# Performance work log

Hardware: AMD Instinct MI355X
Metric: run time of the kernel (lower is better)

Reference implementation:

```python
import jax, jax.numpy as jnp
import numpy as np

ND, NA, E, EL, H, F = 100000, 50000, 500000, 200000, 128, 128


def setup_inputs() -> dict:
    key = jax.random.key(0)
    ks = jax.random.split(key, 20)
    def W(k, shape):
        return jax.random.normal(k, shape, dtype=jnp.float32) * 0.05
    inp = {
        'doc_x': jax.random.normal(ks[0], (ND, F), dtype=jnp.float32),
        'author_node_id': jnp.arange(NA, dtype=jnp.int64 if jax.config.jax_enable_x64 else jnp.int32),
        'edge_index': jnp.stack([
            jax.random.randint(ks[1], (E,), 0, ND),   # doc src
            jax.random.randint(ks[2], (E,), 0, NA),   # author dst
        ]),
        'edge_label_index': jnp.stack([
            jax.random.randint(ks[3], (EL,), 0, ND),
            jax.random.randint(ks[4], (EL,), 0, NA),
        ]),
        'doc_lin_W': W(ks[5], (F, H)), 'doc_lin_b': W(ks[6], (H,)),
        'author_emb': W(ks[7], (NA, H)),
        'c1_da_Wl': W(ks[8], (H, H)), 'c1_da_bl': W(ks[9], (H,)), 'c1_da_Wr': W(ks[10], (H, H)),
        'c1_ad_Wl': W(ks[11], (H, H)), 'c1_ad_bl': W(ks[12], (H,)), 'c1_ad_Wr': W(ks[13], (H, H)),
        'c2_da_Wl': W(ks[14], (H, H)), 'c2_da_bl': W(ks[15], (H,)), 'c2_da_Wr': W(ks[16], (H, H)),
        'c2_ad_Wl': W(ks[17], (H, H)), 'c2_ad_bl': W(ks[18], (H,)), 'c2_ad_Wr': W(ks[19], (H, H)),
    }
    return inp


def sage(x_src, x_dst, src, dst, num_dst, Wl, bl, Wr):
    # PyG SAGEConv (aggr='mean'): lin_l(mean_j x_src[j]) + lin_r(x_dst)
    msg = x_src[src]                                            # [E, H]
    agg = jax.ops.segment_sum(msg, dst, num_segments=num_dst)   # [num_dst, H]
    deg = jax.ops.segment_sum(jnp.ones_like(dst, dtype=x_src.dtype), dst, num_segments=num_dst)
    agg = agg / jnp.maximum(deg, 1.0)[:, None]
    return agg @ Wl + bl + x_dst @ Wr


def reference(doc_x, author_node_id, edge_index, edge_label_index,
              doc_lin_W, doc_lin_b, author_emb,
              c1_da_Wl, c1_da_bl, c1_da_Wr, c1_ad_Wl, c1_ad_bl, c1_ad_Wr,
              c2_da_Wl, c2_da_bl, c2_da_Wr, c2_ad_Wl, c2_ad_bl, c2_ad_Wr):
    x_doc = doc_x @ doc_lin_W + doc_lin_b          # [ND, H]
    x_author = author_emb[author_node_id]          # [NA, H]
    src_d, dst_a = edge_index[0], edge_index[1]
    # layer 1 (per-edge-type convs, to_hetero semantics) + ReLU
    h_a = sage(x_doc, x_author, src_d, dst_a, NA, c1_da_Wl, c1_da_bl, c1_da_Wr)
    h_d = sage(x_author, x_doc, dst_a, src_d, ND, c1_ad_Wl, c1_ad_bl, c1_ad_Wr)
    h_a, h_d = jax.nn.relu(h_a), jax.nn.relu(h_d)
    # layer 2
    o_a = sage(h_d, h_a, src_d, dst_a, NA, c2_da_Wl, c2_da_bl, c2_da_Wr)
    o_d = sage(h_a, h_d, dst_a, src_d, ND, c2_ad_Wl, c2_ad_bl, c2_ad_Wr)
    # edge scorer: dot product of gathered endpoint embeddings
    pred = (o_d[edge_label_index[0]] * o_a[edge_label_index[1]]).sum(-1)  # [EL]
    return pred
```

## Files before the change

kernel.cpp:

```cpp
#include <hip/hip_runtime.h>

typedef unsigned short u16;
typedef __attribute__((ext_vector_type(8))) short vbf16x8;
typedef __attribute__((ext_vector_type(4))) float vf32x4;

__device__ __forceinline__ float bf2f(u16 u) {
    union { unsigned int i; float f; } v; v.i = ((unsigned int)u) << 16; return v.f;
}
__device__ __forceinline__ u16 f2bf(float f) {
    union { float f; unsigned int i; } v; v.f = f;
    return (u16)((v.i + 0x7fffu + ((v.i >> 16) & 1u)) >> 16);
}

struct TPack { const float* src[9]; u16* dst[9]; };

#define NBUK 256
#define NBLK_BIN 256
#define SCAP 24
#define OVFCAP 32768
#define PACK_SH 17

__global__ __launch_bounds__(256) void wtp(TPack p, int* __restrict__ ovfn) {
    int b = blockIdx.x;
    if (b == 0 && threadIdx.x < 2) ovfn[threadIdx.x] = 0;
    int mat = b >> 6;
    const float* s = p.src[mat];
    u16* d = p.dst[mat];
    int i = (b & 63) * 256 + threadIdx.x;
    int k = i >> 7, n = i & 127;
    d[(size_t)n * 128 + k] = f2bf(s[(size_t)k * 128 + n]);
}

__global__ __launch_bounds__(256) void mega2(
    const float* __restrict__ A1f, const u16* __restrict__ W1T,
    const float* __restrict__ biasd, u16* __restrict__ xdoc, int M, int BD,
    const float* __restrict__ emb, const int* __restrict__ ids,
    u16* __restrict__ xauth, int NA, int gatherB,
    const int* __restrict__ src, const int* __restrict__ dst,
    unsigned* __restrict__ stageD, unsigned* __restrict__ stageA,
    int* __restrict__ cntD, int* __restrict__ cntA,
    uint2* __restrict__ ovfD, uint2* __restrict__ ovfA, int* __restrict__ ovfn,
    int E, int shD, int shA) {
    __shared__ u16 WS[128 * 128];
    const int tid = threadIdx.x;

    const long b = blockIdx.x;
    const long nB = 2 * NBLK_BIN;
    const long T = (long)BD + nB + gatherB;
    const long gq0 = (b * BD) / T, gq1 = ((b + 1) * BD) / T;

    if (gq1 > gq0) {
        const int tile = (int)gq0;
        const int lane = tid & 63, wave = tid >> 6;
        const int r15 = lane & 15, kq = lane >> 4;
        const int rowbase = tile * 128 + wave * 32;
        const int m0 = rowbase + r15, m1 = rowbase + 16 + r15;
        const bool v0 = rowbase < M, v1 = rowbase + 16 < M;

        vf32x4 acc0[8], acc1[8];
#pragma unroll
        for (int i = 0; i < 8; ++i) { acc0[i] = (vf32x4)(0.0f); acc1[i] = (vf32x4)(0.0f); }

#pragma unroll
        for (int i = 0; i < 8; ++i) {
            int L = i * 256 + tid;
            int n = L >> 4, bk = L & 15;
            *(uint4*)(WS + ((size_t)n * 16 + (bk ^ (n & 15))) * 8) =
                *(const uint4*)(W1T + (size_t)L * 8);
        }
        __syncthreads();

#pragma unroll
        for (int ks = 0; ks < 4; ++ks) {
            vbf16x8 a0 = (vbf16x8)(short)0, a1 = (vbf16x8)(short)0;
            if (v0) {
                const float* p = A1f + (size_t)m0 * 128 + ks * 32 + kq * 8;
                float4 lo = *(const float4*)p, hi = *(const float4*)(p + 4);
                a0[0] = (short)f2bf(lo.x); a0[1] = (short)f2bf(lo.y);
                a0[2] = (short)f2bf(lo.z); a0[3] = (short)f2bf(lo.w);
                a0[4] = (short)f2bf(hi.x); a0[5] = (short)f2bf(hi.y);
                a0[6] = (short)f2bf(hi.z); a0[7] = (short)f2bf(hi.w);
            }
            if (v1) {
                const float* p = A1f + (size_t)m1 * 128 + ks * 32 + kq * 8;
                float4 lo = *(const float4*)p, hi = *(const float4*)(p + 4);
                a1[0] = (short)f2bf(lo.x); a1[1] = (short)f2bf(lo.y);
                a1[2] = (short)f2bf(lo.z); a1[3] = (short)f2bf(lo.w);
                a1[4] = (short)f2bf(hi.x); a1[5] = (short)f2bf(hi.y);
                a1[6] = (short)f2bf(hi.z); a1[7] = (short)f2bf(hi.w);
            }
#pragma unroll
            for (int nt = 0; nt < 8; ++nt) {
                vbf16x8 bb = *(const vbf16x8*)(
                    WS + ((size_t)(nt * 16 + r15) * 16 + ((ks * 4 + kq) ^ r15)) * 8);
                acc0[nt] = __builtin_amdgcn_mfma_f32_16x16x32_bf16(a0, bb, acc0[nt], 0, 0, 0);
                acc1[nt] = __builtin_amdgcn_mfma_f32_16x16x32_bf16(a1, bb, acc1[nt], 0, 0, 0);
            }
        }

#pragma unroll
        for (int nt = 0; nt < 8; ++nt) {
            const float bv = biasd[nt * 16 + r15];
#pragma unroll
            for (int r = 0; r < 4; ++r) {
                if (v0) xdoc[(size_t)(rowbase + kq * 4 + r) * 128 + nt * 16 + r15] =
                    f2bf(acc0[nt][r] + bv);
                if (v1) xdoc[(size_t)(rowbase + 16 + kq * 4 + r) * 128 + nt * 16 + r15] =
                    f2bf(acc1[nt][r] + bv);
            }
        }
        return;
    }

    const long b2 = b - gq0;
    const long T2 = T - BD;
    const long bq0 = (b2 * nB) / T2, bq1 = ((b2 + 1) * nB) / T2;

    if (bq1 > bq0) {
        int* lcnt = (int*)WS;
        int bb = (int)bq0;
        const bool isD = bb < NBLK_BIN;
        const int blk = isD ? bb : bb - NBLK_BIN;
        const int* key = isD ? src : dst;
        const int* val = isD ? dst : src;
        const int shift = isD ? shD : shA;
        unsigned* stage = isD ? stageD : stageA;
        int* cnt = isD ? cntD : cntA;
        uint2* ovf = isD ? ovfD : ovfA;
        int* on = ovfn + (isD ? 0 : 1);
        const int per = (E + NBLK_BIN - 1) / NBLK_BIN;
        const int beg = blk * per;
        const int end = min(beg + per, E);
        for (int i = tid; i < NBUK; i += 256) lcnt[i] = 0;
        __syncthreads();
        for (int e = beg + tid; e < end; e += 256) {
            int k = key[e], v = val[e];
            int bkt = k >> shift;
            int slot = atomicAdd(&lcnt[bkt], 1);
            if (slot < SCAP) {
                unsigned local = (unsigned)(k - (bkt << shift));
                stage[((size_t)bkt * NBLK_BIN + blk) * SCAP + slot] =
                    (local << PACK_SH) | (unsigned)v;
            } else {
                int oi = atomicAdd(on, 1);
                if (oi < OVFCAP) ovf[oi] = make_uint2((unsigned)k, (unsigned)v);
            }
        }
        __syncthreads();
        for (int i = tid; i < NBUK; i += 256)
            cnt[(size_t)i * NBLK_BIN + blk] = min(lcnt[i], SCAP);
        return;
    }

    int gid = (int)(b2 - bq0) * 256 + tid;
    if (gid >= NA * 16) return;
    int n = gid >> 4, f = gid & 15;
    int id = ids[n];
    const float* s = emb + (size_t)id * 128 + f * 8;
    float4 lo = *(const float4*)(s);
    float4 hi = *(const float4*)(s + 4);
    u16 o[8] = {f2bf(lo.x), f2bf(lo.y), f2bf(lo.z), f2bf(lo.w),
                f2bf(hi.x), f2bf(hi.y), f2bf(hi.z), f2bf(hi.w)};
    *(uint4*)(xauth + (size_t)n * 128 + f * 8) = *(const uint4*)o;
}

__global__ __launch_bounds__(256) void bucket_count2(
    const unsigned* __restrict__ stageD, const unsigned* __restrict__ stageA,
    const int* __restrict__ cntD, const int* __restrict__ cntA,
    const uint2* __restrict__ ovfD, const uint2* __restrict__ ovfA,
    const int* __restrict__ ovfn,
    int* __restrict__ cnt_d, int* __restrict__ cnt_a, int* __restrict__ btot,
    int ND, int NA, int shD, int shA) {
    __shared__ int hist[1024];
    __shared__ int segc[NBLK_BIN];
    __shared__ int red[256];
    const bool isD = (int)blockIdx.x < NBUK;
    const int b = isD ? (int)blockIdx.x : (int)blockIdx.x - NBUK;
    const int sh = isD ? shD : shA;
    const int N = isD ? ND : NA;
    const int base = b << sh;
    const int range = min(1 << sh, N - base);
    const int tid = threadIdx.x;
    if (range <= 0) { if (tid == 0) btot[blockIdx.x] = 0; return; }
    const unsigned* stage = (isD ? stageD : stageA) + (size_t)b * NBLK_BIN * SCAP;
    const int* scnt = (isD ? cntD : cntA) + (size_t)b * NBLK_BIN;
    const uint2* ovf = isD ? ovfD : ovfA;
    const int nov = min(ovfn[isD ? 0 : 1], OVFCAP);
    int* out = isD ? cnt_d : cnt_a;
    for (int i = tid; i < (1 << sh); i += 256) hist[i] = 0;
    segc[tid] = scnt[tid];
    __syncthreads();
    int my = 0;
    for (int j = tid; j < NBLK_BIN * SCAP; j += 256) {
        int seg = j / SCAP, slot = j - seg * SCAP;
        if (slot < segc[seg]) { atomicAdd(&hist[stage[j] >> PACK_SH], 1); ++my; }
    }
    for (int i = tid; i < nov; i += 256) {
        int k = (int)ovf[i].x;
        if ((k >> sh) == b) { atomicAdd(&hist[k - base], 1); ++my; }
    }
    red[tid] = my;
    __syncthreads();
    for (int s = 128; s > 0; s >>= 1) {
        if (tid < s) red[tid] += red[tid + s];
        __syncthreads();
    }
    if (tid == 0) btot[blockIdx.x] = red[0];
    for (int i = tid; i < range; i += 256) out[base + i] = hist[i];
}

__global__ __launch_bounds__(256) void bucket_fill3(
    const unsigned* __restrict__ stageD, const unsigned* __restrict__ stageA,
    const int* __restrict__ cntD, const int* __restrict__ cntA,
    const uint2* __restrict__ ovfD, const uint2* __restrict__ ovfA,
    const int* __restrict__ ovfn,
    const int* __restrict__ cnt_d, const int* __restrict__ cnt_a,
    const int* __restrict__ btot,
    int* __restrict__ offs_d, int* __restrict__ offs_a,
    int* __restrict__ nbr_d, int* __restrict__ nbr_a,
    int ND, int NA, int shD, int shA) {
    __shared__ int lcur[1024];
    __shared__ int segc[NBLK_BIN];
    __shared__ int sh[256];
    __shared__ int carry;
    const bool isD = (int)blockIdx.x < NBUK;
    const int b = isD ? (int)blockIdx.x : (int)blockIdx.x - NBUK;
    const int shft = isD ? shD : shA;
    const int N = isD ? ND : NA;
    const int base = b << shft;
    const int range = min(1 << shft, N - base);
    if (range <= 0) return;
    const unsigned* stage = (isD ? stageD : stageA) + (size_t)b * NBLK_BIN * SCAP;
    const int* scnt = (isD ? cntD : cntA) + (size_t)b * NBLK_BIN;
    const uint2* ovf = isD ? ovfD : ovfA;
    const int nov = min(ovfn[isD ? 0 : 1], OVFCAP);
    const int* cnodes = isD ? cnt_d : cnt_a;
    int* offs = isD ? offs_d : offs_a;
    int* nbr = isD ? nbr_d : nbr_a;
    const int tid = threadIdx.x;
    segc[tid] = scnt[tid];
    {
        const int lo = isD ? 0 : NBUK;
        int acc = 0;
        for (int j = lo + tid; j < (int)blockIdx.x; j += 256) acc += btot[j];
        sh[tid] = acc;
        __syncthreads();
        for (int s = 128; s > 0; s >>= 1) {
            if (tid < s) sh[tid] += sh[tid + s];
            __syncthreads();
        }
        if (tid == 0) carry = sh[0];
        __syncthreads();
    }
    for (int c0 = 0; c0 < range; c0 += 256) {
        int i = c0 + tid;
        int v = (i < range) ? cnodes[base + i] : 0;
        sh[tid] = v;
        __syncthreads();
        for (int off = 1; off < 256; off <<= 1) {
            int t = tid >= off ? sh[tid - off] : 0;
            __syncthreads();
            sh[tid] += t;
            __syncthreads();
        }
        if (i < range) {
            int ex = carry + sh[tid] - v;
            lcur[i] = ex;
            offs[base + i] = ex;
        }
        __syncthreads();
        if (tid == 255) carry += sh[255];
        __syncthreads();
    }
    if (tid == 0) offs[base + range] = carry;
    __syncthreads();
    for (int j = tid; j < NBLK_BIN * SCAP; j += 256) {
        int seg = j / SCAP, slot = j - seg * SCAP;
        if (slot < segc[seg]) {
            unsigned pk = stage[j];
            int local = pk >> PACK_SH;
            int v = (int)(pk & ((1u << PACK_SH) - 1u));
            nbr[atomicAdd(&lcur[local], 1)] = v;
        }
    }
    for (int i = tid; i < nov; i += 256) {
        int k = (int)ovf[i].x;
        if ((k >> shft) == b)
            nbr[atomicAdd(&lcur[k - base], 1)] = (int)ovf[i].y;
    }
}

__global__ __launch_bounds__(256) void agg_mean2(
    const u16* __restrict__ xa, const int* __restrict__ offs_a,
    const int* __restrict__ nbr_a, u16* __restrict__ outa, int NA,
    const u16* __restrict__ xd, const int* __restrict__ offs_d,
    const int* __restrict__ nbr_d, u16* __restrict__ outd, int ND) {
    int gid = blockIdx.x * 256 + threadIdx.x;
    int node = gid >> 4, f = gid & 15;
    int lane = threadIdx.x & 63;
    int gbase = lane & 48;
    const u16* x; const int* offs; const int* nbr; u16* out;
    if (node < NA) { x = xa; offs = offs_a; nbr = nbr_a; out = outa; }
    else {
        node -= NA;
        if (node >= ND) return;
        x = xd; offs = offs_d; nbr = nbr_d; out = outd;
    }
    int beg = offs[node], end = offs[node + 1];
    float acc[8] = {0, 0, 0, 0, 0, 0, 0, 0};

    for (int i = beg; i < end; i += 16) {
        int cnt = end - i; if (cnt > 16) cnt = 16;
        int myn = (i + f < end) ? nbr[i + f] : 0;
        int t = 0;
        for (; t + 3 < cnt; t += 4) {
            int i0 = __shfl(myn, gbase + t);
            int i1 = __shfl(myn, gbase + t + 1);
            int i2 = __shfl(myn, gbase + t + 2);
            int i3 = __shfl(myn, gbase + t + 3);
            uint4 q0 = *(const uint4*)(x + (size_t)i0 * 128 + f * 8);
            uint4 q1 = *(const uint4*)(x + (size_t)i1 * 128 + f * 8);
            uint4 q2 = *(const uint4*)(x + (size_t)i2 * 128 + f * 8);
            uint4 q3 = *(const uint4*)(x + (size_t)i3 * 128 + f * 8);
            acc[0] += bf2f((u16)(q0.x & 0xffff)) + bf2f((u16)(q1.x & 0xffff))
                    + bf2f((u16)(q2.x & 0xffff)) + bf2f((u16)(q3.x & 0xffff));
            acc[1] += bf2f((u16)(q0.x >> 16))    + bf2f((u16)(q1.x >> 16))
                    + bf2f((u16)(q2.x >> 16))    + bf2f((u16)(q3.x >> 16));
            acc[2] += bf2f((u16)(q0.y & 0xffff)) + bf2f((u16)(q1.y & 0xffff))
                    + bf2f((u16)(q2.y & 0xffff)) + bf2f((u16)(q3.y & 0xffff));
            acc[3] += bf2f((u16)(q0.y >> 16))    + bf2f((u16)(q1.y >> 16))
                    + bf2f((u16)(q2.y >> 16))    + bf2f((u16)(q3.y >> 16));
            acc[4] += bf2f((u16)(q0.z & 0xffff)) + bf2f((u16)(q1.z & 0xffff))
                    + bf2f((u16)(q2.z & 0xffff)) + bf2f((u16)(q3.z & 0xffff));
            acc[5] += bf2f((u16)(q0.z >> 16))    + bf2f((u16)(q1.z >> 16))
                    + bf2f((u16)(q2.z >> 16))    + bf2f((u16)(q3.z >> 16));
            acc[6] += bf2f((u16)(q0.w & 0xffff)) + bf2f((u16)(q1.w & 0xffff))
                    + bf2f((u16)(q2.w & 0xffff)) + bf2f((u16)(q3.w & 0xffff));
            acc[7] += bf2f((u16)(q0.w >> 16))    + bf2f((u16)(q1.w >> 16))
                    + bf2f((u16)(q2.w >> 16))    + bf2f((u16)(q3.w >> 16));
        }
        for (; t < cnt; ++t) {
            int i0 = __shfl(myn, gbase + t);
            uint4 q0 = *(const uint4*)(x + (size_t)i0 * 128 + f * 8);
            acc[0] += bf2f((u16)(q0.x & 0xffff));
            acc[1] += bf2f((u16)(q0.x >> 16));
            acc[2] += bf2f((u16)(q0.y & 0xffff));
            acc[3] += bf2f((u16)(q0.y >> 16));
            acc[4] += bf2f((u16)(q0.z & 0xffff));
            acc[5] += bf2f((u16)(q0.z >> 16));
            acc[6] += bf2f((u16)(q0.w & 0xffff));
            acc[7] += bf2f((u16)(q0.w >> 16));
        }
    }
    float inv = 1.0f / fmaxf((float)(end - beg), 1.0f);
    u16 o[8];
#pragma unroll
    for (int j = 0; j < 8; ++j) o[j] = f2bf(acc[j] * inv);
    *(uint4*)(out + (size_t)node * 128 + f * 8) = *(const uint4*)o;
}

struct SideParams3 {
    const u16* A1b; const u16* W1T;
    const u16* A2b; const u16* W2T;
    const float* bias; u16* out;
    int M; int do_relu; int ntiles; int gblocks;
};
__global__ __launch_bounds__(256) void conv_gemm3(SideParams3 sa, SideParams3 sd) {
    __shared__ u16 WS[2 * 128 * 128];
    const bool isA = (int)blockIdx.x < sa.gblocks;
    SideParams3 P = isA ? sa : sd;
    const int gb = isA ? (int)blockIdx.x : (int)blockIdx.x - sa.gblocks;
    const int tid = threadIdx.x;
    const int lane = tid & 63, wave = tid >> 6;
    const int r15 = lane & 15, kq = lane >> 4;

#pragma unroll
    for (int i = 0; i < 8; ++i) {
        int L = i * 256 + tid;
        int n = L >> 4, bk = L & 15;
        *(uint4*)(WS + ((size_t)n * 16 + (bk ^ (n & 15))) * 8) =
            *(const uint4*)(P.W1T + (size_t)L * 8);
        *(uint4*)(WS + 16384 + ((size_t)n * 16 + (bk ^ (n & 15))) * 8) =
            *(const uint4*)(P.W2T + (size_t)L * 8);
    }
    __syncthreads();
    float bv[8];
#pragma unroll
    for (int nt = 0; nt < 8; ++nt) bv[nt] = P.bias[nt * 16 + r15];

    auto loadA = [&](const u16* Ab, int tile, vbf16x8* fa, vbf16x8* fb) {
        const int rowbase = tile * 128 + wave * 32;
        const int m0 = rowbase + r15, m1 = rowbase + 16 + r15;
        const bool v0 = rowbase < P.M, v1 = rowbase + 16 < P.M;
#pragma unroll
        for (int ks = 0; ks < 4; ++ks) {
            fa[ks] = v0 ? *(const vbf16x8*)(Ab + (size_t)m0 * 128 + ks * 32 + kq * 8)
                        : (vbf16x8)(short)0;
            fb[ks] = v1 ? *(const vbf16x8*)(Ab + (size_t)m1 * 128 + ks * 32 + kq * 8)
                        : (vbf16x8)(short)0;
        }
    };

    vbf16x8 c1a[4], c1b[4], c2a[4], c2b[4], n1a[4], n1b[4];
    if (gb < P.ntiles) loadA(P.A1b, gb, c1a, c1b);
    for (int t = gb; t < P.ntiles; t += P.gblocks) {
        loadA(P.A2b, t, c2a, c2b);
        const int tn = t + P.gblocks;
        if (tn < P.ntiles) loadA(P.A1b, tn, n1a, n1b);

        vf32x4 acc0[8], acc1[8];
#pragma unroll
        for (int i = 0; i < 8; ++i) { acc0[i] = (vf32x4)(0.0f); acc1[i] = (vf32x4)(0.0f); }
#pragma unroll
        for (int ks = 0; ks < 4; ++ks) {
#pragma unroll
            for (int nt = 0; nt < 8; ++nt) {
                vbf16x8 b = *(const vbf16x8*)(
                    WS + ((size_t)(nt * 16 + r15) * 16 + ((ks * 4 + kq) ^ r15)) * 8);
                acc0[nt] = __builtin_amdgcn_mfma_f32_16x16x32_bf16(c1a[ks], b, acc0[nt], 0, 0, 0);
                acc1[nt] = __builtin_amdgcn_mfma_f32_16x16x32_bf16(c1b[ks], b, acc1[nt], 0, 0, 0);
            }
        }
#pragma unroll
        for (int ks = 0; ks < 4; ++ks) {
#pragma unroll
            for (int nt = 0; nt < 8; ++nt) {
                vbf16x8 b = *(const vbf16x8*)(
                    WS + 16384 + ((size_t)(nt * 16 + r15) * 16 + ((ks * 4 + kq) ^ r15)) * 8);
                acc0[nt] = __builtin_amdgcn_mfma_f32_16x16x32_bf16(c2a[ks], b, acc0[nt], 0, 0, 0);
                acc1[nt] = __builtin_amdgcn_mfma_f32_16x16x32_bf16(c2b[ks], b, acc1[nt], 0, 0, 0);
            }
        }

        const int rowbase = t * 128 + wave * 32;
        const bool v0 = rowbase < P.M, v1 = rowbase + 16 < P.M;
#pragma unroll
        for (int nt = 0; nt < 8; ++nt) {
#pragma unroll
            for (int r = 0; r < 4; ++r) {
                if (v0) {
                    float v = acc0[nt][r] + bv[nt];
                    if (P.do_relu) v = fmaxf(v, 0.0f);
                    P.out[(size_t)(rowbase + kq * 4 + r) * 128 + nt * 16 + r15] = f2bf(v);
                }
                if (v1) {
                    float v = acc1[nt][r] + bv[nt];
                    if (P.do_relu) v = fmaxf(v, 0.0f);
                    P.out[(size_t)(rowbase + 16 + kq * 4 + r) * 128 + nt * 16 + r15] = f2bf(v);
                }
            }
        }
#pragma unroll
        for (int ks = 0; ks < 4; ++ks) { c1a[ks] = n1a[ks]; c1b[ks] = n1b[ks]; }
    }
}

__global__ __launch_bounds__(256) void edge_dot(
    const u16* __restrict__ od, const u16* __restrict__ oa,
    const int* __restrict__ i0, const int* __restrict__ i1,
    float* __restrict__ pred, int EL) {
    int gid = blockIdx.x * 256 + threadIdx.x;
    if (gid >= EL * 16) return;
    int e = gid >> 4, f = gid & 15;
    uint4 x = *(const uint4*)(od + (size_t)i0[e] * 128 + f * 8);
    uint4 y = *(const uint4*)(oa + (size_t)i1[e] * 128 + f * 8);
    float s = 0.0f;
    s += bf2f((u16)(x.x & 0xffff)) * bf2f((u16)(y.x & 0xffff));
    s += bf2f((u16)(x.x >> 16))    * bf2f((u16)(y.x >> 16));
    s += bf2f((u16)(x.y & 0xffff)) * bf2f((u16)(y.y & 0xffff));
    s += bf2f((u16)(x.y >> 16))    * bf2f((u16)(y.y >> 16));
    s += bf2f((u16)(x.z & 0xffff)) * bf2f((u16)(y.z & 0xffff));
    s += bf2f((u16)(x.z >> 16))    * bf2f((u16)(y.z >> 16));
    s += bf2f((u16)(x.w & 0xffff)) * bf2f((u16)(y.w & 0xffff));
    s += bf2f((u16)(x.w >> 16))    * bf2f((u16)(y.w >> 16));
    s += __shfl_xor(s, 1);
    s += __shfl_xor(s, 2);
    s += __shfl_xor(s, 4);
    s += __shfl_xor(s, 8);
    if (f == 0) pred[e] = s;
}

extern "C" void kernel_launch(void* const* d_in, const int* in_sizes, int n_in,
                              void* d_out, int out_size, void* d_ws, size_t ws_size,
                              hipStream_t stream) {
    const float* doc_x    = (const float*)d_in[0];
    const int*   auth_id  = (const int*)d_in[1];
    const int*   eidx     = (const int*)d_in[2];
    const int*   elidx    = (const int*)d_in[3];
    const float* W_doc    = (const float*)d_in[4];
    const float* b_doc    = (const float*)d_in[5];
    const float* emb      = (const float*)d_in[6];
    const float* c1_da_Wl = (const float*)d_in[7];
    const float* c1_da_bl = (const float*)d_in[8];
    const float* c1_da_Wr = (const float*)d_in[9];
    const float* c1_ad_Wl = (const float*)d_in[10];
    const float* c1_ad_bl = (const float*)d_in[11];
    const float* c1_ad_Wr = (const float*)d_in[12];
    const float* c2_da_Wl = (const float*)d_in[13];
    const float* c2_da_bl = (const float*)d_in[14];
    const float* c2_da_Wr = (const float*)d_in[15];
    const float* c2_ad_Wl = (const float*)d_in[16];
    const float* c2_ad_bl = (const float*)d_in[17];
    const float* c2_ad_Wr = (const float*)d_in[18];

    const int ND = in_sizes[0] / 128;
    const int NA = in_sizes[1];
    const int E  = in_sizes[2] / 2;
    const int EL = in_sizes[3] / 2;
    const int* e_src = eidx;
    const int* e_dst = eidx + E;
    const int BA = (NA + 127) / 128, BD = (ND + 127) / 128;
    const int gatherB = (NA * 16 + 255) / 256;

    char* base = (char*)d_ws;
    size_t off = 0;
    auto alloc = [&](size_t bytes) {
        void* p = base + off;
        off = (off + bytes + 255) & ~(size_t)255;
        return p;
    };
    u16*  xdoc  = (u16*)alloc((size_t)ND * 128 * 2);
    u16*  xauth = (u16*)alloc((size_t)NA * 128 * 2);
    u16*  hd    = (u16*)alloc((size_t)ND * 128 * 2);
    u16*  ha    = (u16*)alloc((size_t)NA * 128 * 2);
    u16*  aggA  = (u16*)alloc((size_t)NA * 128 * 2);
    u16*  aggD  = (u16*)alloc((size_t)ND * 128 * 2);
    u16*  wt    = (u16*)alloc((size_t)9 * 128 * 128 * 2);
    int*  cnt   = (int*)alloc((size_t)(ND + NA) * 4);
    int*  offs_d = (int*)alloc((size_t)(ND + 1) * 4);
    int*  offs_a = (int*)alloc((size_t)(NA + 1) * 4);
    int*  nbr_d = (int*)alloc((size_t)E * 4);
    int*  nbr_a = (int*)alloc((size_t)E * 4);
    int*  cntD  = (int*)alloc((size_t)NBUK * NBLK_BIN * 4);
    int*  cntA  = (int*)alloc((size_t)NBUK * NBLK_BIN * 4);
    int*  btot  = (int*)alloc((size_t)2 * NBUK * 4);
    uint2* ovfD = (uint2*)alloc((size_t)OVFCAP * 8);
    uint2* ovfA = (uint2*)alloc((size_t)OVFCAP * 8);
    int*  ovfn  = (int*)alloc(256);
    (void)ws_size; (void)n_in; (void)out_size;
    u16* od = xdoc;
    u16* oa = xauth;
    unsigned* stageD = (unsigned*)aggD;
    unsigned* stageA = (unsigned*)aggA;

    TPack tp;
    const float* srcs[9] = {W_doc, c1_da_Wl, c1_da_Wr, c1_ad_Wl, c1_ad_Wr,
                            c2_da_Wl, c2_da_Wr, c2_ad_Wl, c2_ad_Wr};
    for (int i = 0; i < 9; ++i) { tp.src[i] = srcs[i]; tp.dst[i] = wt + (size_t)i * 16384; }
    const u16 *WTdoc = wt, *WT_c1daL = wt + 16384, *WT_c1daR = wt + 2 * 16384,
              *WT_c1adL = wt + 3 * 16384, *WT_c1adR = wt + 4 * 16384,
              *WT_c2daL = wt + 5 * 16384, *WT_c2daR = wt + 6 * 16384,
              *WT_c2adL = wt + 7 * 16384, *WT_c2adR = wt + 8 * 16384;

    int shD = 0; while (((ND - 1) >> shD) >= NBUK) ++shD;
    int shA = 0; while (((NA - 1) >> shA) >= NBUK) ++shA;

    wtp<<<576, 256, 0, stream>>>(tp, ovfn);

    mega2<<<BD + 2 * NBLK_BIN + gatherB, 256, 0, stream>>>(
        doc_x, WTdoc, b_doc, xdoc, ND, BD,
        emb, auth_id, xauth, NA, gatherB,
        e_src, e_dst, stageD, stageA, cntD, cntA, ovfD, ovfA, ovfn,
        E, shD, shA);

    bucket_count2<<<2 * NBUK, 256, 0, stream>>>(
        stageD, stageA, cntD, cntA, ovfD, ovfA, ovfn,
        cnt, cnt + ND, btot, ND, NA, shD, shA);

    bucket_fill3<<<2 * NBUK, 256, 0, stream>>>(
        stageD, stageA, cntD, cntA, ovfD, ovfA, ovfn,
        cnt, cnt + ND, btot, offs_d, offs_a, nbr_d, nbr_a,
        ND, NA, shD, shA);

    const int aggGrid = ((NA + ND) * 16 + 255) / 256;
    const int gA = (int)(((long)512 * BA) / (BA + BD));
    const int gD = 512 - gA;

    agg_mean2<<<aggGrid, 256, 0, stream>>>(
        xdoc, offs_a, nbr_a, aggA, NA, xauth, offs_d, nbr_d, aggD, ND);
    {
        SideParams3 sa = {aggA, WT_c1daL, xauth, WT_c1daR, c1_da_bl, ha, NA, 1, BA, gA};
        SideParams3 sd = {aggD, WT_c1adL, xdoc,  WT_c1adR, c1_ad_bl, hd, ND, 1, BD, gD};
        conv_gemm3<<<gA + gD, 256, 0, stream>>>(sa, sd);
    }

    agg_mean2<<<aggGrid, 256, 0, stream>>>(
        hd, offs_a, nbr_a, aggA, NA, ha, offs_d, nbr_d, aggD, ND);
    {
        SideParams3 sa = {aggA, WT_c2daL, ha, WT_c2daR, c2_da_bl, oa, NA, 0, BA, gA};
        SideParams3 sd = {aggD, WT_c2adL, hd, WT_c2adR, c2_ad_bl, od, ND, 0, BD, gD};
        conv_gemm3<<<gA + gD, 256, 0, stream>>>(sa, sd);
    }

    edge_dot<<<(EL * 16 + 255) / 256, 256, 0, stream>>>(
        od, oa, elidx, elidx + EL, (float*)d_out, EL);
}
```

Measured before the change: 360.0 us.

## Interleave per-side aggregation and conv GEMM blocks across staged kernels

Splits the combined aggregation and conv launches into per-side stages and fuses each side's conv with the next side's neighbor aggregation in one launch. Conv blocks and gather blocks are interleaved by block index so memory-bound gathers and MFMA tiles can run at the same time. The conv kernel becomes one tile per block with a single 32KB weight buffer reloaded per matrix, in place of the persistent loop with 64KB of shared memory and register prefetch. This adds a fifth launch, reloads weights for every tile, and drops the cross-tile prefetch in exchange for overlap and lower LDS use.

```diff
diff --git a/kernel.cpp b/kernel.cpp
--- a/kernel.cpp
+++ b/kernel.cpp
@@ -290,28 +290,27 @@
     }
 }
 
-__global__ __launch_bounds__(256) void agg_mean2(
-    const u16* __restrict__ xa, const int* __restrict__ offs_a,
-    const int* __restrict__ nbr_a, u16* __restrict__ outa, int NA,
-    const u16* __restrict__ xd, const int* __restrict__ offs_d,
-    const int* __restrict__ nbr_d, u16* __restrict__ outd, int ND) {
-    int gid = blockIdx.x * 256 + threadIdx.x;
-    int node = gid >> 4, f = gid & 15;
-    int lane = threadIdx.x & 63;
+struct AggP { const u16* x; const int* offs; const int* nbr; u16* out; int N; };
+struct ConvP {
+    const u16* A1b; const u16* W1T;
+    const u16* A2b; const u16* W2T;
+    const float* bias; u16* out;
+    int M; int do_relu; int ntiles;
+};
+
+__device__ __forceinline__ void agg_block(const AggP& A, int blk, int tid) {
+    int node = blk * 16 + (tid >> 4);
+    int f = tid & 15;
+    if (node >= A.N) return;
+    int lane = tid & 63;
     int gbase = lane & 48;
-    const u16* x; const int* offs; const int* nbr; u16* out;
-    if (node < NA) { x = xa; offs = offs_a; nbr = nbr_a; out = outa; }
-    else {
-        node -= NA;
-        if (node >= ND) return;
-        x = xd; offs = offs_d; nbr = nbr_d; out = outd;
-    }
-    int beg = offs[node], end = offs[node + 1];
+    const u16* x = A.x;
+    int beg = A.offs[node], end = A.offs[node + 1];
     float acc[8] = {0, 0, 0, 0, 0, 0, 0, 0};
 
     for (int i = beg; i < end; i += 16) {
         int cnt = end - i; if (cnt > 16) cnt = 16;
-        int myn = (i + f < end) ? nbr[i + f] : 0;
+        int myn = (i + f < end) ? A.nbr[i + f] : 0;
         int t = 0;
         for (; t + 3 < cnt; t += 4) {
             int i0 = __shfl(myn, gbase + t);
@@ -356,103 +355,84 @@
     u16 o[8];
 #pragma unroll
     for (int j = 0; j < 8; ++j) o[j] = f2bf(acc[j] * inv);
-    *(uint4*)(out + (size_t)node * 128 + f * 8) = *(const uint4*)o;
-}
-
-struct SideParams3 {
-    const u16* A1b; const u16* W1T;
-    const u16* A2b; const u16* W2T;
-    const float* bias; u16* out;
-    int M; int do_relu; int ntiles; int gblocks;
-};
-__global__ __launch_bounds__(256) void conv_gemm3(SideParams3 sa, SideParams3 sd) {
-    __shared__ u16 WS[2 * 128 * 128];
-    const bool isA = (int)blockIdx.x < sa.gblocks;
-    SideParams3 P = isA ? sa : sd;
-    const int gb = isA ? (int)blockIdx.x : (int)blockIdx.x - sa.gblocks;
-    const int tid = threadIdx.x;
+    *(uint4*)(A.out + (size_t)node * 128 + f * 8) = *(const uint4*)o;
+}
+
+__device__ __forceinline__ void conv_tile(const ConvP& P, int bx, u16* WS, int tid) {
     const int lane = tid & 63, wave = tid >> 6;
     const int r15 = lane & 15, kq = lane >> 4;
-
-#pragma unroll
-    for (int i = 0; i < 8; ++i) {
-        int L = i * 256 + tid;
-        int n = L >> 4, bk = L & 15;
-        *(uint4*)(WS + ((size_t)n * 16 + (bk ^ (n & 15))) * 8) =
-            *(const uint4*)(P.W1T + (size_t)L * 8);
-        *(uint4*)(WS + 16384 + ((size_t)n * 16 + (bk ^ (n & 15))) * 8) =
-            *(const uint4*)(P.W2T + (size_t)L * 8);
-    }
-    __syncthreads();
-    float bv[8];
-#pragma unroll
-    for (int nt = 0; nt < 8; ++nt) bv[nt] = P.bias[nt * 16 + r15];
-
-    auto loadA = [&](const u16* Ab, int tile, vbf16x8* fa, vbf16x8* fb) {
-        const int rowbase = tile * 128 + wave * 32;
-        const int m0 = rowbase + r15, m1 = rowbase + 16 + r15;
-        const bool v0 = rowbase < P.M, v1 = rowbase + 16 < P.M;
+    const int rowbase = bx * 128 + wave * 32;
+    const int m0 = rowbase + r15, m1 = rowbase + 16 + r15;
+    const bool v0 = rowbase < P.M, v1 = rowbase + 16 < P.M;
+
+    vf32x4 acc0[8], acc1[8];
+#pragma unroll
+    for (int i = 0; i < 8; ++i) { acc0[i] = (vf32x4)(0.0f); acc1[i] = (vf32x4)(0.0f); }
+
+#pragma unroll
+    for (int mat = 0; mat < 2; ++mat) {
+        const u16* WT = mat ? P.W2T : P.W1T;
+        if (mat) __syncthreads();
+#pragma unroll
+        for (int i = 0; i < 8; ++i) {
+            int L = i * 256 + tid;
+            int n = L >> 4, bk = L & 15;
+            *(uint4*)(WS + ((size_t)n * 16 + (bk ^ (n & 15))) * 8) =
+                *(const uint4*)(WT + (size_t)L * 8);
+        }
+        __syncthreads();
+
+        const u16* Ab = mat ? P.A2b : P.A1b;
 #pragma unroll
         for (int ks = 0; ks < 4; ++ks) {
-            fa[ks] = v0 ? *(const vbf16x8*)(Ab + (size_t)m0 * 128 + ks * 32 + kq * 8)
-                        : (vbf16x8)(short)0;
-            fb[ks] = v1 ? *(const vbf16x8*)(Ab + (size_t)m1 * 128 + ks * 32 + kq * 8)
-                        : (vbf16x8)(short)0;
-        }
-    };
-
-    vbf16x8 c1a[4], c1b[4], c2a[4], c2b[4], n1a[4], n1b[4];
-    if (gb < P.ntiles) loadA(P.A1b, gb, c1a, c1b);
-    for (int t = gb; t < P.ntiles; t += P.gblocks) {
-        loadA(P.A2b, t, c2a, c2b);
-        const int tn = t + P.gblocks;
-        if (tn < P.ntiles) loadA(P.A1b, tn, n1a, n1b);
-
-        vf32x4 acc0[8], acc1[8];
-#pragma unroll
-        for (int i = 0; i < 8; ++i) { acc0[i] = (vf32x4)(0.0f); acc1[i] = (vf32x4)(0.0f); }
-#pragma unroll
-        for (int ks = 0; ks < 4; ++ks) {
+            vbf16x8 a0 = (vbf16x8)(short)0, a1 = (vbf16x8)(short)0;
+            if (v0) a0 = *(const vbf16x8*)(Ab + (size_t)m0 * 128 + ks * 32 + kq * 8);
+            if (v1) a1 = *(const vbf16x8*)(Ab + (size_t)m1 * 128 + ks * 32 + kq * 8);
 #pragma unroll
             for (int nt = 0; nt < 8; ++nt) {
                 vbf16x8 b = *(const vbf16x8*)(
                     WS + ((size_t)(nt * 16 + r15) * 16 + ((ks * 4 + kq) ^ r15)) * 8);
-                acc0[nt] = __builtin_amdgcn_mfma_f32_16x16x32_bf16(c1a[ks], b, acc0[nt], 0, 0, 0);
-                acc1[nt] = __builtin_amdgcn_mfma_f32_16x16x32_bf16(c1b[ks], b, acc1[nt], 0, 0, 0);
-            }
-        }
-#pragma unroll
-        for (int ks = 0; ks < 4; ++ks) {
-#pragma unroll
-            for (int nt = 0; nt < 8; ++nt) {
-                vbf16x8 b = *(const vbf16x8*)(
-                    WS + 16384 + ((size_t)(nt * 16 + r15) * 16 + ((ks * 4 + kq) ^ r15)) * 8);
-                acc0[nt] = __builtin_amdgcn_mfma_f32_16x16x32_bf16(c2a[ks], b, acc0[nt], 0, 0, 0);
-                acc1[nt] = __builtin_amdgcn_mfma_f32_16x16x32_bf16(c2b[ks], b, acc1[nt], 0, 0, 0);
-            }
-        }
-
-        const int rowbase = t * 128 + wave * 32;
-        const bool v0 = rowbase < P.M, v1 = rowbase + 16 < P.M;
-#pragma unroll
-        for (int nt = 0; nt < 8; ++nt) {
-#pragma unroll
-            for (int r = 0; r < 4; ++r) {
-                if (v0) {
-                    float v = acc0[nt][r] + bv[nt];
-                    if (P.do_relu) v = fmaxf(v, 0.0f);
-                    P.out[(size_t)(rowbase + kq * 4 + r) * 128 + nt * 16 + r15] = f2bf(v);
-                }
-                if (v1) {
-                    float v = acc1[nt][r] + bv[nt];
-                    if (P.do_relu) v = fmaxf(v, 0.0f);
-                    P.out[(size_t)(rowbase + 16 + kq * 4 + r) * 128 + nt * 16 + r15] = f2bf(v);
-                }
-            }
-        }
-#pragma unroll
-        for (int ks = 0; ks < 4; ++ks) { c1a[ks] = n1a[ks]; c1b[ks] = n1b[ks]; }
-    }
+                acc0[nt] = __builtin_amdgcn_mfma_f32_16x16x32_bf16(a0, b, acc0[nt], 0, 0, 0);
+                acc1[nt] = __builtin_amdgcn_mfma_f32_16x16x32_bf16(a1, b, acc1[nt], 0, 0, 0);
+            }
+        }
+    }
+
+#pragma unroll
+    for (int nt = 0; nt < 8; ++nt) {
+        const float bv = P.bias[nt * 16 + r15];
+#pragma unroll
+        for (int r = 0; r < 4; ++r) {
+            if (v0) {
+                float v = acc0[nt][r] + bv;
+                if (P.do_relu) v = fmaxf(v, 0.0f);
+                P.out[(size_t)(rowbase + kq * 4 + r) * 128 + nt * 16 + r15] = f2bf(v);
+            }
+            if (v1) {
+                float v = acc1[nt][r] + bv;
+                if (P.do_relu) v = fmaxf(v, 0.0f);
+                P.out[(size_t)(rowbase + 16 + kq * 4 + r) * 128 + nt * 16 + r15] = f2bf(v);
+            }
+        }
+    }
+}
+
+__global__ __launch_bounds__(256) void agg_side(AggP A) {
+    agg_block(A, blockIdx.x, threadIdx.x);
+}
+__global__ __launch_bounds__(256) void conv_side(ConvP C) {
+    __shared__ u16 WS[128 * 128];
+    conv_tile(C, blockIdx.x, WS, threadIdx.x);
+}
+
+__global__ __launch_bounds__(256) void aggconv(AggP A, int naggB, ConvP C) {
+    __shared__ u16 WS[128 * 128];
+    const long b = blockIdx.x;
+    const long nc = C.ntiles;
+    const long T = (long)naggB + nc;
+    const long c0 = (b * nc) / T, c1 = ((b + 1) * nc) / T;
+    if (c1 > c0) conv_tile(C, (int)c0, WS, threadIdx.x);
+    else         agg_block(A, (int)(b - c0), threadIdx.x);
 }
 
 __global__ __launch_bounds__(256) void edge_dot(
@@ -511,6 +491,8 @@
     const int* e_dst = eidx + E;
     const int BA = (NA + 127) / 128, BD = (ND + 127) / 128;
     const int gatherB = (NA * 16 + 255) / 256;
+    const int aggBA = (NA * 16 + 255) / 256;
+    const int aggBD = (ND * 16 + 255) / 256;
 
     char* base = (char*)d_ws;
     size_t off = 0;
@@ -523,8 +505,8 @@
     u16*  xauth = (u16*)alloc((size_t)NA * 128 * 2);
     u16*  hd    = (u16*)alloc((size_t)ND * 128 * 2);
     u16*  ha    = (u16*)alloc((size_t)NA * 128 * 2);
-    u16*  aggA  = (u16*)alloc((size_t)NA * 128 * 2);
-    u16*  aggD  = (u16*)alloc((size_t)ND * 128 * 2);
+    u16*  agg1  = (u16*)alloc((size_t)ND * 128 * 2);
+    u16*  agg2  = (u16*)alloc((size_t)ND * 128 * 2);
     u16*  wt    = (u16*)alloc((size_t)9 * 128 * 128 * 2);
     int*  cnt   = (int*)alloc((size_t)(ND + NA) * 4);
     int*  offs_d = (int*)alloc((size_t)(ND + 1) * 4);
@@ -540,8 +522,8 @@
     (void)ws_size; (void)n_in; (void)out_size;
     u16* od = xdoc;
     u16* oa = xauth;
-    unsigned* stageD = (unsigned*)aggD;
-    unsigned* stageA = (unsigned*)aggA;
+    unsigned* stageD = (unsigned*)agg1;
+    unsigned* stageA = (unsigned*)agg2;
 
     TPack tp;
     const float* srcs[9] = {W_doc, c1_da_Wl, c1_da_Wr, c1_ad_Wl, c1_ad_Wr,
@@ -572,24 +554,32 @@
         cnt, cnt + ND, btot, offs_d, offs_a, nbr_d, nbr_a,
         ND, NA, shD, shA);
 
-    const int aggGrid = ((NA + ND) * 16 + 255) / 256;
-    const int gA = (int)(((long)512 * BA) / (BA + BD));
-    const int gD = 512 - gA;
-
-    agg_mean2<<<aggGrid, 256, 0, stream>>>(
-        xdoc, offs_a, nbr_a, aggA, NA, xauth, offs_d, nbr_d, aggD, ND);
     {
-        SideParams3 sa = {aggA, WT_c1daL, xauth, WT_c1daR, c1_da_bl, ha, NA, 1, BA, gA};
-        SideParams3 sd = {aggD, WT_c1adL, xdoc,  WT_c1adR, c1_ad_bl, hd, ND, 1, BD, gD};
-        conv_gemm3<<<gA + gD, 256, 0, stream>>>(sa, sd);
-    }
-
-    agg_mean2<<<aggGrid, 256, 0, stream>>>(
-        hd, offs_a, nbr_a, aggA, NA, ha, offs_d, nbr_d, aggD, ND);
+        AggP A = {xdoc, offs_a, nbr_a, agg1, NA};
+        agg_side<<<aggBA, 256, 0, stream>>>(A);
+    }
+
     {
-        SideParams3 sa = {aggA, WT_c2daL, ha, WT_c2daR, c2_da_bl, oa, NA, 0, BA, gA};
-        SideParams3 sd = {aggD, WT_c2adL, hd, WT_c2adR, c2_ad_bl, od, ND, 0, BD, gD};
-        conv_gemm3<<<gA + gD, 256, 0, stream>>>(sa, sd);
+        AggP A = {xauth, offs_d, nbr_d, agg2, ND};
+        ConvP C = {agg1, WT_c1daL, xauth, WT_c1daR, c1_da_bl, ha, NA, 1, BA};
+        aggconv<<<aggBD + BA, 256, 0, stream>>>(A, aggBD, C);
+    }
+
+    {
+        AggP A = {ha, offs_d, nbr_d, agg1, ND};
+        ConvP C = {agg2, WT_c1adL, xdoc, WT_c1adR, c1_ad_bl, hd, ND, 1, BD};
+        aggconv<<<aggBD + BD, 256, 0, stream>>>(A, aggBD, C);
+    }
+
+    {
+        AggP A = {hd, offs_a, nbr_a, agg2, NA};
+        ConvP C = {agg1, WT_c2adL, hd, WT_c2adR, c2_ad_bl, od, ND, 0, BD};
+        aggconv<<<aggBA + BD, 256, 0, stream>>>(A, aggBA, C);
+    }
+
+    {
+        ConvP C = {agg2, WT_c2daL, ha, WT_c2daR, c2_da_bl, oa, NA, 0, BA};
+        conv_side<<<BA, 256, 0, stream>>>(C);
     }
 
     edge_dot<<<(EL * 16 + 255) / 256, 256, 0, stream>>>(
```

After: 430.6 us. 19.6% more time.
